# Kernel tuning notes

Measured on AMD Instinct MI355X. Metric: run time of the kernel, lower is better.

The kernel has to match this reference:

```python
import jax, jax.numpy as jnp
import numpy as np

B, S, D, H = 2, 2048, 2048, 16
HD = D // H            # 128
BLK = 16               # sparsity block size
LOCAL = 4              # num_local_blocks
GLOBAL = 1             # num_global_blocks
ROPE_THETA = 10000.0


def _fixed_layout(num_blocks: int) -> np.ndarray:
    """DeepSpeed FixedSparsityConfig block layout (unidirectional,
    different_layout_per_head=False, num_different_global_patterns=1,
    horizontal_global_attention=False)."""
    layout = np.zeros((num_blocks, num_blocks), dtype=bool)
    # local windows of LOCAL blocks, causal at block granularity inside window
    for w in range(0, num_blocks, LOCAL):
        end = min(w + LOCAL, num_blocks)
        for row in range(w, end):
            layout[row, w:row + 1] = True
    # vertical global columns: last GLOBAL block(s) of each window
    first = LOCAL - GLOBAL  # head % num_different_global_patterns == 0
    stop = num_blocks - (num_blocks % LOCAL)
    for i in range(first, stop, LOCAL):
        layout[i:, i:i + GLOBAL] = True  # unidirectional: rows >= i
    return layout

_LAYOUT = _fixed_layout(S // BLK)  # [num_blocks, num_blocks] bool, static


def _rope(t, cos, sin):
    # t: [B, S, H, HD]; pairs are adjacent (llama complex view)
    tr = t.reshape(B, S, H, HD // 2, 2)
    a, b = tr[..., 0], tr[..., 1]
    c = cos[None, :, None, :]
    s = sin[None, :, None, :]
    out = jnp.stack([a * c - b * s, a * s + b * c], axis=-1)
    return out.reshape(B, S, H, HD)


def setup_inputs() -> dict:
    key = jax.random.key(0)
    kx, kq, kk, kv, ko = jax.random.split(key, 5)
    x = jax.random.normal(kx, (B, S, D), dtype=jnp.float32)
    wscale = 1.0 / np.sqrt(D)
    wq = jax.random.normal(kq, (D, D), dtype=jnp.float32) * wscale
    wk = jax.random.normal(kk, (D, D), dtype=jnp.float32) * wscale
    wv = jax.random.normal(kv, (D, D), dtype=jnp.float32) * wscale
    wo = jax.random.normal(ko, (D, D), dtype=jnp.float32) * wscale
    # rotary tables (freqs_cis split into real/imag parts)
    freqs = 1.0 / (ROPE_THETA ** (np.arange(0, HD, 2, dtype=np.float32) / HD))
    angles = np.arange(S, dtype=np.float32)[:, None] * freqs[None, :]  # [S, HD//2]
    cos = jnp.asarray(np.cos(angles), dtype=jnp.float32)
    sin = jnp.asarray(np.sin(angles), dtype=jnp.float32)
    return {"x": x, "cos": cos, "sin": sin, "wq": wq, "wk": wk, "wv": wv, "wo": wo}


def reference(x, cos, sin, wq, wk, wv, wo):
    xq = (x @ wq).reshape(B, S, H, HD)
    xk = (x @ wk).reshape(B, S, H, HD)
    xv = (x @ wv).reshape(B, S, H, HD)
    xq = _rope(xq, cos, sin)
    xk = _rope(xk, cos, sin)
    # module casts q/k/v to fp16 before the sparse kernel; emulate precision
    xq = xq.astype(jnp.float16).astype(jnp.float32)
    xk = xk.astype(jnp.float16).astype(jnp.float32)
    xv = xv.astype(jnp.float16).astype(jnp.float32)
    q = jnp.transpose(xq, (0, 2, 1, 3))  # [B, H, S, HD]
    k = jnp.transpose(xk, (0, 2, 1, 3))
    v = jnp.transpose(xv, (0, 2, 1, 3))
    scale = 1.0 / np.sqrt(HD)
    scores = jnp.einsum('bhqd,bhkd->bhqk', q, k) * scale
    # block-granularity sparsity mask (DeepSpeed masks only at block level)
    blk = jnp.arange(S) // BLK
    mask = jnp.asarray(_LAYOUT)[blk[:, None], blk[None, :]]  # [S, S] bool
    scores = jnp.where(mask[None, None], scores, -jnp.inf)
    probs = jax.nn.softmax(scores, axis=-1)
    out = jnp.einsum('bhqk,bhkd->bhqd', probs, v)  # [B, H, S, HD]
    out = jnp.transpose(out, (0, 2, 1, 3)).reshape(B, S, D)
    return out @ wo
```

## Files before the change

kernel.cpp:

```cpp
#include <hip/hip_runtime.h>

#define B_ 2
#define S_ 2048
#define D_ 2048
#define H_ 16
#define HD_ 128

typedef _Float16 fp16x2 __attribute__((ext_vector_type(2)));
typedef _Float16 fp16x4 __attribute__((ext_vector_type(4)));
typedef _Float16 fp16x8 __attribute__((ext_vector_type(8)));
typedef float f32x4 __attribute__((ext_vector_type(4)));

__device__ __forceinline__ void gl_lds16(const _Float16* g, _Float16* l) {
  __builtin_amdgcn_global_load_lds((const __attribute__((address_space(1))) void*)g,
                                   (__attribute__((address_space(3))) void*)l, 16, 0, 0);
}

__global__ __launch_bounds__(256) void k_cast(const float* __restrict__ in,
                                              _Float16* __restrict__ out, int n4) {
  int i = blockIdx.x * 256 + threadIdx.x;
  if (i >= n4) return;
  f32x4 v = ((const f32x4*)in)[i];
  fp16x4 h = {(_Float16)v[0], (_Float16)v[1], (_Float16)v[2], (_Float16)v[3]};
  ((fp16x4*)out)[i] = h;
}

__global__ __launch_bounds__(256) void k_trw4(const float* __restrict__ w0,
                                              const float* __restrict__ w1,
                                              const float* __restrict__ w2,
                                              const float* __restrict__ w3,
                                              _Float16* __restrict__ o0,
                                              _Float16* __restrict__ o1,
                                              _Float16* __restrict__ o2,
                                              _Float16* __restrict__ o3) {
  __shared__ float tile[64][65];
  const float* w = (blockIdx.z == 0) ? w0 : (blockIdx.z == 1) ? w1 : (blockIdx.z == 2) ? w2 : w3;
  _Float16* wt = (blockIdx.z == 0) ? o0 : (blockIdx.z == 1) ? o1 : (blockIdx.z == 2) ? o2 : o3;
  int k0 = blockIdx.y * 64, n0 = blockIdx.x * 64;
  int t = threadIdx.x;
  int r = t >> 2, c0 = (t & 3) * 16;
  const float* ip = w + (size_t)(k0 + r) * D_ + n0 + c0;
#pragma unroll
  for (int j = 0; j < 16; j += 4) {
    f32x4 v = *(const f32x4*)(ip + j);
    tile[r][c0 + j] = v[0]; tile[r][c0 + j + 1] = v[1];
    tile[r][c0 + j + 2] = v[2]; tile[r][c0 + j + 3] = v[3];
  }
  __syncthreads();
  _Float16* op = wt + (size_t)(n0 + r) * D_ + k0 + c0;
#pragma unroll
  for (int j = 0; j < 16; j += 8) {
    fp16x8 v;
#pragma unroll
    for (int q = 0; q < 8; ++q) v[q] = (_Float16)tile[c0 + j + q][r];
    *(fp16x8*)(op + j) = v;
  }
}

template <int MODE>
__global__ __launch_bounds__(512) void k_gemm256(const _Float16* __restrict__ A,
                                                 const _Float16* __restrict__ BT,
                                                 const float* __restrict__ cosT,
                                                 const float* __restrict__ sinT,
                                                 _Float16* __restrict__ Qo,
                                                 _Float16* __restrict__ Ko,
                                                 _Float16* __restrict__ Vo,
                                                 float* __restrict__ Cf) {
  __shared__ __align__(16) _Float16 smem[73728];
  const int tid = threadIdx.x;
  const int w = tid >> 6, lane = tid & 63;
  const int l15 = lane & 15, lg = lane >> 4;
  const int NPX = (MODE == 0) ? 6 : 2;
  const int bid = blockIdx.x;
  const int xcd = bid & 7, j = bid >> 3;
  const int m0 = (j / NPX) * 256;
  const int n0 = (xcd * NPX + j % NPX) * 128;
  const int wm = (w >> 1) * 64;
  const int wn = (w & 1) * 64;
  const int lr = lane >> 3, lc = lane & 7;
  const int scol = (lc ^ lr) << 3;
  const _Float16* Asrc = A + (size_t)(m0 + w * 8 + lr) * 2048 + scol;
  const _Float16* Bsrc = BT + (size_t)(n0 + w * 8 + lr) * 2048 + scol;
  _Float16* dstA = smem + w * 512;
  _Float16* dstB = smem + 49152 + w * 512;

  auto stageA = [&](int stg, int u, int k0) {
    gl_lds16(Asrc + (size_t)u * 64 * 2048 + k0, dstA + stg * 16384 + u * 4096);
  };
  auto stageB = [&](int stg, int u, int k0) {
    gl_lds16(Bsrc + (size_t)u * 64 * 2048 + k0, dstB + stg * 8192 + u * 4096);
  };

  int aoff[4], boff[4];
#pragma unroll
  for (int mi = 0; mi < 4; ++mi) {
    const int row = wm + mi * 16 + l15;
    aoff[mi] = (row >> 6) * 4096 + (row & 63) * 64;
  }
#pragma unroll
  for (int ni = 0; ni < 4; ++ni) {
    const int row = wn + ni * 16 + l15;
    boff[ni] = (row >> 6) * 4096 + (row & 63) * 64;
  }
  const int swz[2] = {(lg * 8) ^ ((l15 & 7) * 8), (32 + lg * 8) ^ ((l15 & 7) * 8)};

  f32x4 acc[4][4] = {};

#pragma unroll
  for (int u = 0; u < 4; ++u) stageA(0, u, 0);
  stageB(0, 0, 0); stageB(0, 1, 0);
#pragma unroll
  for (int u = 0; u < 4; ++u) stageA(1, u, 64);
  stageB(1, 0, 64); stageB(1, 1, 64);
  asm volatile("s_waitcnt vmcnt(6)" ::: "memory");
  __builtin_amdgcn_s_barrier();

  for (int t = 0; t < 32; ++t) {
    const int cur = t % 3;
    const bool pf = (t + 2) < 32;
    const int spf = (t + 2) % 3, kpf = (t + 2) * 64;
    const _Float16* sA = smem + cur * 16384;
    const _Float16* sB = smem + 49152 + cur * 8192;
#pragma unroll
    for (int ks = 0; ks < 2; ++ks) {
      fp16x8 af[4], bf[4];
#pragma unroll
      for (int mi = 0; mi < 4; ++mi) af[mi] = *(const fp16x8*)(sA + aoff[mi] + swz[ks]);
#pragma unroll
      for (int ni = 0; ni < 4; ++ni) bf[ni] = *(const fp16x8*)(sB + boff[ni] + swz[ks]);
      if (ks == 0) {
        if (pf) { stageA(spf, 0, kpf); stageA(spf, 1, kpf); stageA(spf, 2, kpf); }
      } else {
        if (pf) {
          stageA(spf, 3, kpf); stageB(spf, 0, kpf); stageB(spf, 1, kpf);
          asm volatile("s_waitcnt vmcnt(6)" ::: "memory");
        } else {
          asm volatile("s_waitcnt vmcnt(0)" ::: "memory");
        }
      }
      __builtin_amdgcn_s_barrier();
      asm volatile("s_waitcnt lgkmcnt(0)" ::: "memory");
      __builtin_amdgcn_s_setprio(1);
#pragma unroll
      for (int mi = 0; mi < 4; ++mi)
#pragma unroll
        for (int ni = 0; ni < 4; ++ni)
          acc[mi][ni] = __builtin_amdgcn_mfma_f32_16x16x32_f16(af[mi], bf[ni],
                                                               acc[mi][ni], 0, 0, 0);
      __builtin_amdgcn_s_setprio(0);
      __builtin_amdgcn_s_barrier();
    }
  }

  if (MODE == 0) {
    const int region = n0 >> 11;
    if (region < 2) {
      _Float16* Out = (region == 0) ? Qo : Ko;
#pragma unroll
      for (int mi = 0; mi < 4; ++mi)
#pragma unroll
        for (int ni = 0; ni < 4; ++ni) {
          const int col = n0 + wn + 16 * ni + l15;
          const int d = col & 127;
          const int h = (col >> 7) & 15;
          const int dp = d >> 1;
          const bool odd = d & 1;
#pragma unroll
          for (int i = 0; i < 4; ++i) {
            const int row = m0 + wm + 16 * mi + 4 * lg + i;
            const int b = row >> 11, sl = row & 2047;
            const float self = acc[mi][ni][i];
            const float partner = __shfl_xor(self, 1);
            const float c = cosT[sl * 64 + dp], sn = sinT[sl * 64 + dp];
            const float val = odd ? (partner * sn + self * c) : (self * c - partner * sn);
            Out[(((size_t)b * H_ + h) * S_ + sl) * HD_ + d] = (_Float16)val;
          }
        }
    } else {
#pragma unroll
      for (int mi = 0; mi < 4; ++mi)
#pragma unroll
        for (int ni = 0; ni < 4; ++ni) {
          const int col = n0 + wn + 16 * ni + l15;
          const int d = col & 127;
          const int h = (col >> 7) & 15;
          const int row0 = m0 + wm + 16 * mi + 4 * lg;
          const int b = row0 >> 11, sl0 = row0 & 2047;
          const int kb = sl0 >> 4, kin = sl0 & 15;
          fp16x4 v4;
#pragma unroll
          for (int i = 0; i < 4; ++i) v4[i] = (_Float16)acc[mi][ni][i];
          *(fp16x4*)(Vo + ((((size_t)b * H_ + h) * 128 + kb) * 128 + d) * 16 + kin) = v4;
        }
    }
  } else {
#pragma unroll
    for (int mi = 0; mi < 4; ++mi)
#pragma unroll
      for (int ni = 0; ni < 4; ++ni) {
        const size_t row = m0 + wm + 16 * mi + 4 * lg;
        const size_t col = n0 + wn + 16 * ni + l15;
#pragma unroll
        for (int i = 0; i < 4; ++i)
          Cf[(row + i) * 2048 + col] = acc[mi][ni][i];
      }
  }
}

__global__ __launch_bounds__(256) void k_attn(const _Float16* __restrict__ Q,
                                              const _Float16* __restrict__ K,
                                              const _Float16* __restrict__ Vb,
                                              _Float16* __restrict__ Oa) {
  __shared__ __align__(16) _Float16 sK[2][2][2048];
  __shared__ __align__(16) _Float16 sV[2][2][2048];
  const int p = blockIdx.x;
  const int qgA = 31 - p, qgB = p;
  const int hh = blockIdx.y, b = blockIdx.z;
  const int t = threadIdx.x;
  const int w = t >> 6, lane = t & 63;
  const int l15 = lane & 15, lg = lane >> 4, g4 = lg * 4;
  const size_t bh = (size_t)b * H_ + hh;
  const float scale = 0.08838834764831845f;

  const int qbA = 4 * qgA + w, qbB = 4 * qgB + w;
  const int LA = qgA + 4, LB = qgB + 4;
  const int nchA = (LA + 1) >> 1, nchB = (LB + 1) >> 1;
  const int total = nchA + nchB;

  const _Float16* QpA = Q + (bh * S_ + (size_t)qbA * 16 + l15) * HD_ + lg * 8;
  const _Float16* QpB = Q + (bh * S_ + (size_t)qbB * 16 + l15) * HD_ + lg * 8;
  fp16x8 qfA[4], qfB[4];
#pragma unroll
  for (int dd = 0; dd < 4; ++dd) {
    qfA[dd] = *(const fp16x8*)(QpA + dd * 32);
    qfB[dd] = *(const fp16x8*)(QpB + dd * 32);
  }
  f32x4 o[8] = {};
  float mrun = -3.0e38f, lsum = 0.f;

  const int sr = t >> 4, sc = t & 15;
  const int ksrc_off = sr * 128 + (sc ^ (sr & 7)) * 8;
  const _Float16* Kb_g = K + bh * S_ * HD_;
  const _Float16* Vb_g = Vb + bh * (size_t)(128 * 2048);

  auto kbof = [&](int qg, int idx) { return idx < qg ? 4 * idx + 3 : 3 * qg + idx; };
  auto chunk_kbs = [&](int ci, int& kb0, int& kb1) {
    int qg, cil;
    if (ci < nchA) { qg = qgA; cil = ci; } else { qg = qgB; cil = ci - nchA; }
    const int L = qg + 4;
    const int i0 = 2 * cil, i1 = i0 + 1;
    kb0 = kbof(qg, i0);
    kb1 = (i1 < L) ? kbof(qg, i1) : kb0;
  };
  auto stage = [&](int buf, int ci) {
    int kb0, kb1;
    chunk_kbs(ci, kb0, kb1);
    gl_lds16(Kb_g + (size_t)kb0 * 2048 + ksrc_off, &sK[buf][0][w * 512]);
    gl_lds16(Kb_g + (size_t)kb1 * 2048 + ksrc_off, &sK[buf][1][w * 512]);
    gl_lds16(Vb_g + (size_t)kb0 * 2048 + t * 8, &sV[buf][0][w * 512]);
    gl_lds16(Vb_g + (size_t)kb1 * 2048 + t * 8, &sV[buf][1][w * 512]);
  };
  auto flush = [&](int qb) {
    const float inv = 1.f / lsum;
    f32x4 li;
#pragma unroll
    for (int i = 0; i < 4; ++i) li[i] = __shfl(inv, g4 + i);
    _Float16* Op = Oa + ((size_t)b * S_ + (size_t)qb * 16 + g4) * D_ + (size_t)hh * HD_ + l15;
#pragma unroll
    for (int ni = 0; ni < 8; ++ni)
#pragma unroll
      for (int i = 0; i < 4; ++i)
        Op[(size_t)i * D_ + 16 * ni] = (_Float16)(o[ni][i] * li[i]);
  };

  stage(0, 0);

  for (int ci = 0; ci < total; ++ci) {
    const int cur = ci & 1;
    if (ci == nchA) {
      flush(qbA);
#pragma unroll
      for (int ni = 0; ni < 8; ++ni) o[ni] = f32x4{0.f, 0.f, 0.f, 0.f};
      mrun = -3.0e38f;
      lsum = 0.f;
    }
    if (ci + 1 < total) {
      stage(cur ^ 1, ci + 1);
      asm volatile("s_waitcnt vmcnt(4)" ::: "memory");
    } else {
      asm volatile("s_waitcnt vmcnt(0)" ::: "memory");
    }
    __builtin_amdgcn_s_barrier();

    const bool inA = ci < nchA;
    const int qg = inA ? qgA : qgB;
    const int qb = inA ? qbA : qbB;
    const int cil = inA ? ci : ci - nchA;
    const int L = qg + 4;
    int kb0, kb1;
    chunk_kbs(ci, kb0, kb1);
    const bool v0 = kb0 <= qb;
    const bool v1 = (2 * cil + 1 < L) && (kb1 <= qb);
    f32x4 st[2];
    const float in0 = v0 ? 0.f : -1.0e30f, in1 = v1 ? 0.f : -1.0e30f;
    st[0] = f32x4{in0, in0, in0, in0};
    st[1] = f32x4{in1, in1, in1, in1};

    const char* kl = (const char*)&sK[cur][0][0];
    const int krow = l15 * 256;
#pragma unroll
    for (int dd = 0; dd < 4; ++dd) {
      const int co = ((dd * 4 + lg) ^ (l15 & 7)) * 16;
      fp16x8 k0 = *(const fp16x8*)(kl + krow + co);
      fp16x8 k1 = *(const fp16x8*)(kl + 4096 + krow + co);
      const fp16x8 qf = inA ? qfA[dd] : qfB[dd];
      st[0] = __builtin_amdgcn_mfma_f32_16x16x32_f16(k0, qf, st[0], 0, 0, 0);
      st[1] = __builtin_amdgcn_mfma_f32_16x16x32_f16(k1, qf, st[1], 0, 0, 0);
    }
    float bm = -3.0e38f;
#pragma unroll
    for (int j = 0; j < 2; ++j)
#pragma unroll
      for (int i = 0; i < 4; ++i) {
        st[j][i] *= scale;
        bm = fmaxf(bm, st[j][i]);
      }
    bm = fmaxf(bm, __shfl_xor(bm, 16));
    bm = fmaxf(bm, __shfl_xor(bm, 32));
    const float mnew = fmaxf(mrun, bm);
    const float corr = __expf(mrun - mnew);
    float pr[2][4];
    float ps = 0.f;
#pragma unroll
    for (int j = 0; j < 2; ++j)
#pragma unroll
      for (int i = 0; i < 4; ++i) {
        pr[j][i] = __expf(st[j][i] - mnew);
        ps += pr[j][i];
      }
    ps += __shfl_xor(ps, 16);
    ps += __shfl_xor(ps, 32);
    lsum = lsum * corr + ps;
    mrun = mnew;
    f32x4 c4;
#pragma unroll
    for (int i = 0; i < 4; ++i) c4[i] = __shfl(corr, g4 + i);
#pragma unroll
    for (int ni = 0; ni < 8; ++ni) {
      o[ni][0] *= c4[0]; o[ni][1] *= c4[1]; o[ni][2] *= c4[2]; o[ni][3] *= c4[3];
    }
    fp16x4 ph0 = {(_Float16)pr[0][0], (_Float16)pr[0][1], (_Float16)pr[0][2], (_Float16)pr[0][3]};
    fp16x4 ph1 = {(_Float16)pr[1][0], (_Float16)pr[1][1], (_Float16)pr[1][2], (_Float16)pr[1][3]};
    const char* vl = (const char*)&sV[cur][0][0];
#pragma unroll
    for (int ni = 0; ni < 8; ++ni) {
      const int vo = (16 * ni + l15) * 32 + g4 * 2;
      fp16x4 vv0 = *(const fp16x4*)(vl + vo);
      fp16x4 vv1 = *(const fp16x4*)(vl + 4096 + vo);
      o[ni] = __builtin_amdgcn_mfma_f32_16x16x16f16(ph0, vv0, o[ni], 0, 0, 0);
      o[ni] = __builtin_amdgcn_mfma_f32_16x16x16f16(ph1, vv1, o[ni], 0, 0, 0);
    }
    __builtin_amdgcn_s_barrier();
  }

  flush(qbB);
}

extern "C" void kernel_launch(void* const* d_in, const int* in_sizes, int n_in,
                              void* d_out, int out_size, void* d_ws, size_t ws_size,
                              hipStream_t stream) {
  const float* x = (const float*)d_in[0];
  const float* cosT = (const float*)d_in[1];
  const float* sinT = (const float*)d_in[2];
  const float* wq = (const float*)d_in[3];
  const float* wk = (const float*)d_in[4];
  const float* wv = (const float*)d_in[5];
  const float* wo = (const float*)d_in[6];
  float* out = (float*)d_out;
  char* ws = (char*)d_ws;

  _Float16* x16 = (_Float16*)(ws);
  _Float16* wtq = (_Float16*)(ws + (16ull << 20));
  _Float16* wtk = (_Float16*)(ws + (24ull << 20));
  _Float16* wtv = (_Float16*)(ws + (32ull << 20));
  _Float16* wto = (_Float16*)(ws + (40ull << 20));
  _Float16* Q16 = (_Float16*)(ws + (48ull << 20));
  _Float16* K16 = (_Float16*)(ws + (64ull << 20));
  _Float16* Vb16 = (_Float16*)(ws + (80ull << 20));

  k_cast<<<8192, 256, 0, stream>>>(x, x16, (B_ * S_ * D_) / 4);
  k_trw4<<<dim3(32, 32, 4), 256, 0, stream>>>(wq, wk, wv, wo, wtq, wtk, wtv, wto);

  k_gemm256<0><<<768, 512, 0, stream>>>(x16, wtq, cosT, sinT, Q16, K16, Vb16, nullptr);

  _Float16* attn16 = x16;
  k_attn<<<dim3(16, H_, B_), 256, 0, stream>>>(Q16, K16, Vb16, attn16);

  k_gemm256<1><<<256, 512, 0, stream>>>(attn16, wto, nullptr, nullptr, nullptr, nullptr,
                                        nullptr, out);
}
```

Before: 225.2 us.

## Use 256x256 tiles with double-buffered pipeline for the fused QKV GEMM

Splits the templated GEMM into a dedicated QKV kernel using 256x256 output tiles (8 waves each computing 128x64) with a simpler two-stage double buffer. This halves the grid from 768 to 384 blocks and raises per-block arithmetic intensity, cutting redundant A/B loads. It also drops an explicit lgkmcnt wait in the output-projection GEMM. The cost is higher register pressure (32 accumulators per wave), a less overlapped prefetch with a full vmcnt(0) wait each step, and 384 blocks on 256 CUs, which leaves a partial second wave.

```diff
diff --git a/kernel.cpp b/kernel.cpp
--- a/kernel.cpp
+++ b/kernel.cpp
@@ -57,20 +57,143 @@
   }
 }
 
-template <int MODE>
-__global__ __launch_bounds__(512) void k_gemm256(const _Float16* __restrict__ A,
+__global__ __launch_bounds__(512) void k_qkv256(const _Float16* __restrict__ A,
+                                                const _Float16* __restrict__ BT,
+                                                const float* __restrict__ cosT,
+                                                const float* __restrict__ sinT,
+                                                _Float16* __restrict__ Qo,
+                                                _Float16* __restrict__ Ko,
+                                                _Float16* __restrict__ Vo) {
+  __shared__ __align__(16) _Float16 smem[65536];
+  const int tid = threadIdx.x;
+  const int w = tid >> 6, lane = tid & 63;
+  const int l15 = lane & 15, lg = lane >> 4;
+  const int bid = blockIdx.x;
+  const int xcd = bid & 7, j = bid >> 3;
+  const int m0 = (j / 3) * 256;
+  const int n0 = (xcd * 3 + j % 3) * 256;
+  const int wm = (w >> 2) * 128;
+  const int wn = (w & 3) * 64;
+  const int lr = lane >> 3, lc = lane & 7;
+  const int scol = (lc ^ lr) << 3;
+  const _Float16* Asrc = A + (size_t)(m0 + w * 8 + lr) * 2048 + scol;
+  const _Float16* Bsrc = BT + (size_t)(n0 + w * 8 + lr) * 2048 + scol;
+  _Float16* dstA = smem + w * 512;
+  _Float16* dstB = smem + 32768 + w * 512;
+
+  auto stageA = [&](int stg, int u, int k0) {
+    gl_lds16(Asrc + (size_t)u * 64 * 2048 + k0, dstA + stg * 16384 + u * 4096);
+  };
+  auto stageB = [&](int stg, int u, int k0) {
+    gl_lds16(Bsrc + (size_t)u * 64 * 2048 + k0, dstB + stg * 16384 + u * 4096);
+  };
+
+  int aoff[8], boff[4];
+#pragma unroll
+  for (int mi = 0; mi < 8; ++mi) {
+    const int r = wm + mi * 16 + l15;
+    aoff[mi] = (r >> 6) * 4096 + (r & 63) * 64;
+  }
+#pragma unroll
+  for (int ni = 0; ni < 4; ++ni) {
+    const int r = wn + ni * 16 + l15;
+    boff[ni] = (r >> 6) * 4096 + (r & 63) * 64;
+  }
+  const int swz[2] = {(lg * 8) ^ ((l15 & 7) * 8), (32 + lg * 8) ^ ((l15 & 7) * 8)};
+
+  f32x4 acc[8][4] = {};
+
+#pragma unroll
+  for (int u = 0; u < 4; ++u) stageA(0, u, 0);
+#pragma unroll
+  for (int u = 0; u < 4; ++u) stageB(0, u, 0);
+
+  for (int t = 0; t < 32; ++t) {
+    const int cur = t & 1, nxt = cur ^ 1;
+    asm volatile("s_waitcnt vmcnt(0)" ::: "memory");
+    __builtin_amdgcn_s_barrier();
+    const bool pf = (t + 1) < 32;
+    const int k1 = (t + 1) * 64;
+    const _Float16* sA = smem + cur * 16384;
+    const _Float16* sB = smem + 32768 + cur * 16384;
+#pragma unroll
+    for (int ks = 0; ks < 2; ++ks) {
+      fp16x8 af[8], bf[4];
+#pragma unroll
+      for (int mi = 0; mi < 8; ++mi) af[mi] = *(const fp16x8*)(sA + aoff[mi] + swz[ks]);
+#pragma unroll
+      for (int ni = 0; ni < 4; ++ni) bf[ni] = *(const fp16x8*)(sB + boff[ni] + swz[ks]);
+      if (pf) {
+        if (ks == 0) {
+#pragma unroll
+          for (int u = 0; u < 4; ++u) stageA(nxt, u, k1);
+        } else {
+#pragma unroll
+          for (int u = 0; u < 4; ++u) stageB(nxt, u, k1);
+        }
+      }
+      __builtin_amdgcn_s_setprio(1);
+#pragma unroll
+      for (int mi = 0; mi < 8; ++mi)
+#pragma unroll
+        for (int ni = 0; ni < 4; ++ni)
+          acc[mi][ni] = __builtin_amdgcn_mfma_f32_16x16x32_f16(af[mi], bf[ni],
+                                                               acc[mi][ni], 0, 0, 0);
+      __builtin_amdgcn_s_setprio(0);
+    }
+    __builtin_amdgcn_s_barrier();
+  }
+
+  const int region = n0 >> 11;
+  if (region < 2) {
+    _Float16* Out = (region == 0) ? Qo : Ko;
+#pragma unroll
+    for (int mi = 0; mi < 8; ++mi)
+#pragma unroll
+      for (int ni = 0; ni < 4; ++ni) {
+        const int col = n0 + wn + 16 * ni + l15;
+        const int d = col & 127;
+        const int h = (col >> 7) & 15;
+        const int dp = d >> 1;
+        const bool odd = d & 1;
+#pragma unroll
+        for (int i = 0; i < 4; ++i) {
+          const int row = m0 + wm + 16 * mi + 4 * lg + i;
+          const int b = row >> 11, sl = row & 2047;
+          const float self = acc[mi][ni][i];
+          const float partner = __shfl_xor(self, 1);
+          const float c = cosT[sl * 64 + dp], sn = sinT[sl * 64 + dp];
+          const float val = odd ? (partner * sn + self * c) : (self * c - partner * sn);
+          Out[(((size_t)b * H_ + h) * S_ + sl) * HD_ + d] = (_Float16)val;
+        }
+      }
+  } else {
+#pragma unroll
+    for (int mi = 0; mi < 8; ++mi)
+#pragma unroll
+      for (int ni = 0; ni < 4; ++ni) {
+        const int col = n0 + wn + 16 * ni + l15;
+        const int d = col & 127;
+        const int h = (col >> 7) & 15;
+        const int row0 = m0 + wm + 16 * mi + 4 * lg;
+        const int b = row0 >> 11, sl0 = row0 & 2047;
+        const int kb = sl0 >> 4, kin = sl0 & 15;
+        fp16x4 v4;
+#pragma unroll
+        for (int i = 0; i < 4; ++i) v4[i] = (_Float16)acc[mi][ni][i];
+        *(fp16x4*)(Vo + ((((size_t)b * H_ + h) * 128 + kb) * 128 + d) * 16 + kin) = v4;
+      }
+  }
+}
+
+__global__ __launch_bounds__(512) void k_gemm_wo(const _Float16* __restrict__ A,
                                                  const _Float16* __restrict__ BT,
-                                                 const float* __restrict__ cosT,
-                                                 const float* __restrict__ sinT,
-                                                 _Float16* __restrict__ Qo,
-                                                 _Float16* __restrict__ Ko,
-                                                 _Float16* __restrict__ Vo,
                                                  float* __restrict__ Cf) {
   __shared__ __align__(16) _Float16 smem[73728];
   const int tid = threadIdx.x;
   const int w = tid >> 6, lane = tid & 63;
   const int l15 = lane & 15, lg = lane >> 4;
-  const int NPX = (MODE == 0) ? 6 : 2;
+  const int NPX = 2;
   const int bid = blockIdx.x;
   const int xcd = bid & 7, j = bid >> 3;
   const int m0 = (j / NPX) * 256;
@@ -139,7 +262,6 @@
         }
       }
       __builtin_amdgcn_s_barrier();
-      asm volatile("s_waitcnt lgkmcnt(0)" ::: "memory");
       __builtin_amdgcn_s_setprio(1);
 #pragma unroll
       for (int mi = 0; mi < 4; ++mi)
@@ -152,59 +274,16 @@
     }
   }
 
-  if (MODE == 0) {
-    const int region = n0 >> 11;
-    if (region < 2) {
-      _Float16* Out = (region == 0) ? Qo : Ko;
-#pragma unroll
-      for (int mi = 0; mi < 4; ++mi)
-#pragma unroll
-        for (int ni = 0; ni < 4; ++ni) {
-          const int col = n0 + wn + 16 * ni + l15;
-          const int d = col & 127;
-          const int h = (col >> 7) & 15;
-          const int dp = d >> 1;
-          const bool odd = d & 1;
-#pragma unroll
-          for (int i = 0; i < 4; ++i) {
-            const int row = m0 + wm + 16 * mi + 4 * lg + i;
-            const int b = row >> 11, sl = row & 2047;
-            const float self = acc[mi][ni][i];
-            const float partner = __shfl_xor(self, 1);
-            const float c = cosT[sl * 64 + dp], sn = sinT[sl * 64 + dp];
-            const float val = odd ? (partner * sn + self * c) : (self * c - partner * sn);
-            Out[(((size_t)b * H_ + h) * S_ + sl) * HD_ + d] = (_Float16)val;
-          }
-        }
-    } else {
-#pragma unroll
-      for (int mi = 0; mi < 4; ++mi)
-#pragma unroll
-        for (int ni = 0; ni < 4; ++ni) {
-          const int col = n0 + wn + 16 * ni + l15;
-          const int d = col & 127;
-          const int h = (col >> 7) & 15;
-          const int row0 = m0 + wm + 16 * mi + 4 * lg;
-          const int b = row0 >> 11, sl0 = row0 & 2047;
-          const int kb = sl0 >> 4, kin = sl0 & 15;
-          fp16x4 v4;
-#pragma unroll
-          for (int i = 0; i < 4; ++i) v4[i] = (_Float16)acc[mi][ni][i];
-          *(fp16x4*)(Vo + ((((size_t)b * H_ + h) * 128 + kb) * 128 + d) * 16 + kin) = v4;
-        }
-    }
-  } else {
-#pragma unroll
-    for (int mi = 0; mi < 4; ++mi)
-#pragma unroll
-      for (int ni = 0; ni < 4; ++ni) {
-        const size_t row = m0 + wm + 16 * mi + 4 * lg;
-        const size_t col = n0 + wn + 16 * ni + l15;
-#pragma unroll
-        for (int i = 0; i < 4; ++i)
-          Cf[(row + i) * 2048 + col] = acc[mi][ni][i];
-      }
-  }
+#pragma unroll
+  for (int mi = 0; mi < 4; ++mi)
+#pragma unroll
+    for (int ni = 0; ni < 4; ++ni) {
+      const size_t row = m0 + wm + 16 * mi + 4 * lg;
+      const size_t col = n0 + wn + 16 * ni + l15;
+#pragma unroll
+      for (int i = 0; i < 4; ++i)
+        Cf[(row + i) * 2048 + col] = acc[mi][ni][i];
+    }
 }
 
 __global__ __launch_bounds__(256) void k_attn(const _Float16* __restrict__ Q,
@@ -391,11 +470,10 @@
   k_cast<<<8192, 256, 0, stream>>>(x, x16, (B_ * S_ * D_) / 4);
   k_trw4<<<dim3(32, 32, 4), 256, 0, stream>>>(wq, wk, wv, wo, wtq, wtk, wtv, wto);
 
-  k_gemm256<0><<<768, 512, 0, stream>>>(x16, wtq, cosT, sinT, Q16, K16, Vb16, nullptr);
+  k_qkv256<<<384, 512, 0, stream>>>(x16, wtq, cosT, sinT, Q16, K16, Vb16);
 
   _Float16* attn16 = x16;
   k_attn<<<dim3(16, H_, B_), 256, 0, stream>>>(Q16, K16, Vb16, attn16);
 
-  k_gemm256<1><<<256, 512, 0, stream>>>(attn16, wto, nullptr, nullptr, nullptr, nullptr,
-                                        nullptr, out);
-}
+  k_gemm_wo<<<256, 512, 0, stream>>>(attn16, wto, out);
+}
```

Result: no change. 224.0 us (-0.5%).
